# Kernel optimization log

Hardware: AMD Instinct MI355X
Metric: run time of the kernel (lower is better)

## Reference

```python
import jax, jax.numpy as jnp
import numpy as np

N_USER, N_ITEM, N_BUNDLE = 200000, 100000, 50000
EMBED_DIM = 128
B, L = 8192, 100  # batch of bundles, max items per bundle


def setup_inputs() -> dict:
    key = jax.random.key(0)
    ks = jax.random.split(key, 12)
    d, d2 = EMBED_DIM, 2 * EMBED_DIM
    x_u = jax.random.randint(ks[0], (B,), 0, N_USER)
    x_b = jax.random.randint(ks[1], (B,), 0, N_BUNDLE)
    items = jax.random.randint(ks[2], (B, L), 0, N_ITEM)
    # ragged bundle sizes in [10, L]; padded+masked form of the CSR gather
    lengths = jax.random.randint(ks[3], (B,), 10, L + 1)
    mask = jnp.arange(L)[None, :] < lengths[:, None]  # [B, L] bool
    return {
        "x_u": x_u,
        "x_b": x_b,
        "items": items,
        "mask": mask,
        "emb_u": jax.random.normal(ks[4], (N_USER, d), jnp.float32) * 0.1,
        "emb_i": jax.random.normal(ks[5], (N_ITEM, d), jnp.float32) * 0.1,
        "emb_b": jax.random.normal(ks[6], (N_BUNDLE, d), jnp.float32) * 0.1,
        "A": jax.random.normal(ks[7], (N_ITEM, d), jnp.float32) * 0.1,
        "fc1_w": jax.random.normal(ks[8], (d2, d2), jnp.float32) / np.sqrt(d2),
        "fc1_b": jnp.zeros((d2,), jnp.float32),
        "fc2_w": jax.random.normal(ks[9], (d2, d2), jnp.float32) / np.sqrt(d2),
        "fc2_b": jnp.zeros((d2,), jnp.float32),
        "out_w": jax.random.normal(ks[10], (1, d2), jnp.float32) / np.sqrt(d2),
        "out_b": jnp.zeros((1,), jnp.float32),
    }


def reference(x_u, x_b, items, mask, emb_u, emb_i, emb_b, A,
              fc1_w, fc1_b, fc2_w, fc2_b, out_w, out_b):
    # DAM.forward_bundle with the attention() per-bundle loop vectorized
    h_u = emb_u[x_u]                       # [B, d]
    h_b = emb_b[x_b]                       # [B, d]
    item_e = emb_i[items]                  # [B, L, d] ragged gather (padded)
    a_e = A[items]                         # [B, L, d]
    # w = softmax_l( sum_d e_u * A[item] ) per bundle, over valid items only
    scores = jnp.einsum('bd,bld->bl', h_u, a_e)
    scores = jnp.where(mask, scores, -jnp.inf)
    w = jax.nn.softmax(scores, axis=1)     # [B, L]
    h_x = jnp.einsum('bl,bld->bd', w, item_e)
    h = jnp.concatenate([h_u, h_b + h_x], axis=1)   # [B, 2d]
    h = jax.nn.leaky_relu(h @ fc1_w.T + fc1_b)
    h = jax.nn.leaky_relu(h @ fc2_w.T + fc2_b)
    return h @ out_w.T + out_b             # [B, 1]
```

## Files before the change

kernel.cpp:

```cpp
#include <hip/hip_runtime.h>
#include <hip/hip_bf16.h>

#define D   128
#define D2  256
#define XS  264
#define H1P 272

typedef short bf16x8 __attribute__((ext_vector_type(8)));
typedef float f32x4  __attribute__((ext_vector_type(4)));

__device__ __forceinline__ float bf2f(unsigned short u) {
    return __uint_as_float(((unsigned int)u) << 16);
}
__device__ __forceinline__ float bflo(unsigned int p) { return __uint_as_float(p << 16); }
__device__ __forceinline__ float bfhi(unsigned int p) { return __uint_as_float(p & 0xffff0000u); }
__device__ __forceinline__ unsigned short f2bf(float f) {
    __hip_bfloat16 h = __float2bfloat16(f);
    return *(unsigned short*)&h;
}

template<bool BF>
__device__ __forceinline__ float ld1(const void* p, size_t i) {
    if constexpr (BF) return bf2f(((const unsigned short*)p)[i]);
    else              return ((const float*)p)[i];
}

template<bool BF>
__device__ __forceinline__ void load8f(const void* p, size_t elem_off, float* r) {
    if constexpr (BF) {
        uint4 v = *(const uint4*)((const unsigned short*)p + elem_off);
        r[0]=bflo(v.x); r[1]=bfhi(v.x); r[2]=bflo(v.y); r[3]=bfhi(v.y);
        r[4]=bflo(v.z); r[5]=bfhi(v.z); r[6]=bflo(v.w); r[7]=bfhi(v.w);
    } else {
        const float4* q = (const float4*)((const float*)p + elem_off);
        float4 a = q[0], b = q[1];
        r[0]=a.x; r[1]=a.y; r[2]=a.z; r[3]=a.w;
        r[4]=b.x; r[5]=b.y; r[6]=b.z; r[7]=b.w;
    }
}

__device__ __forceinline__ void unpack8(uint4 v, float* r) {
    r[0]=bflo(v.x); r[1]=bfhi(v.x); r[2]=bflo(v.y); r[3]=bfhi(v.y);
    r[4]=bflo(v.z); r[5]=bfhi(v.z); r[6]=bflo(v.w); r[7]=bfhi(v.w);
}

__device__ __forceinline__ void store8bf(unsigned short* p, const float* r) {
    union { unsigned short u[8]; uint4 v; } pk;
    #pragma unroll
    for (int k = 0; k < 8; ++k) pk.u[k] = f2bf(r[k]);
    *(uint4*)p = pk.v;
}

__device__ __forceinline__ bool read_mask(const void* mask, int mmode, size_t i) {
    if (mmode == 0) return ((const int*)mask)[i] != 0;
    if (mmode == 1) return ((const unsigned char*)mask)[i] != 0;
    return ((const unsigned short*)mask)[i] != 0;
}

__device__ __forceinline__ bool probe_is_bf16(const unsigned int* probe) {
    const int lane = threadIdx.x & 63;
    int cnt = 0;
    #pragma unroll
    for (int i = 0; i < 4; ++i) {
        unsigned int e = (probe[lane + 64 * i] >> 7) & 0xffu;
        cnt += (e >= 90 && e < 130) ? 1 : 0;
    }
    #pragma unroll
    for (int o = 32; o; o >>= 1) cnt += __shfl_xor(cnt, o);
    return cnt >= 128;
}

template<bool BF>
__device__ __forceinline__ void attn_one_row(
    const int* __restrict__ x_u, const int* __restrict__ x_b,
    const int* __restrict__ items, const void* __restrict__ mask, int mmode,
    const void* __restrict__ emb_u, const void* __restrict__ emb_i,
    const void* __restrict__ emb_b, const void* __restrict__ Aw,
    unsigned short* __restrict__ x_row, int b, int L)
{
    const int lane = threadIdx.x & 63;
    const int xu = x_u[b];

    const int  c0 = (lane < L) ? lane : 0;
    int  i0 = items[(size_t)b * L + c0];
    bool v0 = (lane < L) && read_mask(mask, mmode, (size_t)b * L + c0);
    int  i1 = i0;
    bool v1 = false;
    if (64 + lane < L) {
        i1 = items[(size_t)b * L + 64 + lane];
        v1 = read_mask(mask, mmode, (size_t)b * L + 64 + lane);
    }
    const int len = __popcll(__ballot(v0)) + __popcll(__ballot(v1));

    const int g = lane >> 4, m16 = lane & 15;

    float hu8[8];
    load8f<BF>(emb_u, (size_t)xu * D + m16 * 8, hu8);

    auto get_id = [&](int p) -> int {
        const int idx = 4 * p + g;
        const int src = (idx < len) ? idx : 0;
        return (src < 64) ? __shfl(i0, src) : __shfl(i1, src - 64);
    };

    float esum = 0.f;
    float acc8[8];
    #pragma unroll
    for (int k = 0; k < 8; ++k) acc8[k] = 0.f;

    if constexpr (BF) {
        const unsigned short* AW = (const unsigned short*)Aw;
        const unsigned short* EI = (const unsigned short*)emb_i;
        for (int grp = 0; grp < 4; ++grp) {
            if (grp == 0 || grp * 32 < len) {
                uint4 ab[8], vb[8];
                #pragma unroll
                for (int q = 0; q < 8; ++q) {
                    const int id = get_id(grp * 8 + q);
                    ab[q] = *(const uint4*)(AW + (size_t)id * D + m16 * 8);
                    vb[q] = *(const uint4*)(EI + (size_t)id * D + m16 * 8);
                }
                #pragma unroll
                for (int q = 0; q < 8; ++q) {
                    float af[8];
                    unpack8(ab[q], af);
                    float s = 0.f;
                    #pragma unroll
                    for (int k = 0; k < 8; ++k) s += hu8[k] * af[k];
                    s += __shfl_xor(s, 1); s += __shfl_xor(s, 2);
                    s += __shfl_xor(s, 4); s += __shfl_xor(s, 8);
                    const int idx = 4 * (grp * 8 + q) + g;
                    const float e = (idx < len) ? __expf(s) : 0.f;
                    esum += e;
                    float vf[8];
                    unpack8(vb[q], vf);
                    #pragma unroll
                    for (int k = 0; k < 8; ++k) acc8[k] += e * vf[k];
                }
            }
        }
    } else {
        const int NP = (len + 3) >> 2;
        auto fetchf = [&](int p, float* a, float* v) {
            const int id = get_id(p);
            load8f<false>(Aw,    (size_t)id * D + m16 * 8, a);
            load8f<false>(emb_i, (size_t)id * D + m16 * 8, v);
        };
        float a0[8], u0[8], a1[8], u1[8];
        fetchf(0, a0, u0);
        if (1 < NP) fetchf(1, a1, u1);
        for (int p = 0; p < NP; ++p) {
            float ca[8], cv[8];
            #pragma unroll
            for (int k = 0; k < 8; ++k) { ca[k] = a0[k]; cv[k] = u0[k]; }
            #pragma unroll
            for (int k = 0; k < 8; ++k) { a0[k] = a1[k]; u0[k] = u1[k]; }
            if (p + 2 < NP) fetchf(p + 2, a1, u1);
            float s = 0.f;
            #pragma unroll
            for (int k = 0; k < 8; ++k) s += hu8[k] * ca[k];
            s += __shfl_xor(s, 1); s += __shfl_xor(s, 2);
            s += __shfl_xor(s, 4); s += __shfl_xor(s, 8);
            const int idx = 4 * p + g;
            const float e = (idx < len) ? __expf(s) : 0.f;
            esum += e;
            #pragma unroll
            for (int k = 0; k < 8; ++k) acc8[k] += e * cv[k];
        }
    }

    esum += __shfl_xor(esum, 16);
    esum += __shfl_xor(esum, 32);
    #pragma unroll
    for (int k = 0; k < 8; ++k) {
        acc8[k] += __shfl_xor(acc8[k], 16);
        acc8[k] += __shfl_xor(acc8[k], 32);
    }
    const float inv = (esum > 0.f) ? 1.f / esum : 0.f;

    if (g == 0) {
        if constexpr (BF) {
            uint4 raw = *(const uint4*)((const unsigned short*)emb_u
                                        + (size_t)xu * D + m16 * 8);
            *(uint4*)(x_row + m16 * 8) = raw;
        } else {
            float r[8];
            load8f<false>(emb_u, (size_t)xu * D + m16 * 8, r);
            store8bf(x_row + m16 * 8, r);
        }
        const int xb = x_b[b];
        float rb2[8], outv[8];
        load8f<BF>(emb_b, (size_t)xb * D + m16 * 8, rb2);
        #pragma unroll
        for (int k = 0; k < 8; ++k) outv[k] = rb2[k] + acc8[k] * inv;
        store8bf(x_row + D + m16 * 8, outv);
    }
}

template<bool BF>
__device__ __forceinline__ bf16x8 load_w8(const void* W, size_t off) {
    if constexpr (BF) {
        return *(const bf16x8*)((const unsigned short*)W + off);
    } else {
        const float* p = (const float*)W + off;
        float4 a = *(const float4*)p;
        float4 b = *(const float4*)(p + 4);
        bf16x8 r;
        r[0] = (short)f2bf(a.x); r[1] = (short)f2bf(a.y);
        r[2] = (short)f2bf(a.z); r[3] = (short)f2bf(a.w);
        r[4] = (short)f2bf(b.x); r[5] = (short)f2bf(b.y);
        r[6] = (short)f2bf(b.z); r[7] = (short)f2bf(b.w);
        return r;
    }
}

template<bool BF>
__device__ __forceinline__ void fused_body(
    const int* __restrict__ x_u, const int* __restrict__ x_b,
    const int* __restrict__ items, const void* __restrict__ mask, int mmode,
    const void* __restrict__ emb_u, const void* __restrict__ emb_i,
    const void* __restrict__ emb_b, const void* __restrict__ Aw,
    const void* __restrict__ fc1_w, const void* __restrict__ fc1_b,
    const void* __restrict__ fc2_w, const void* __restrict__ fc2_b,
    const void* __restrict__ out_w, const void* __restrict__ out_b,
    void* __restrict__ out, int L,
    unsigned short* x_s, unsigned short* h1_s, float (*po_s)[16])
{
    const int tid  = threadIdx.x;
    const int wave = tid >> 6;
    const int lane = tid & 63;
    const int l16  = lane & 15;
    const int quad = lane >> 4;
    const int mt   = blockIdx.x * 16;

    #pragma unroll
    for (int rr = 0; rr < 2; ++rr) {
        const int r = wave + rr * 8;
        attn_one_row<BF>(x_u, x_b, items, mask, mmode, emb_u, emb_i, emb_b, Aw,
                         &x_s[r * XS], mt + r, L);
    }
    __syncthreads();

    bf16x8 afrag[8];
    #pragma unroll
    for (int kc = 0; kc < 8; ++kc)
        afrag[kc] = *(const bf16x8*)&x_s[l16 * XS + quad * 8 + kc * 32];

    #pragma unroll
    for (int jj = 0; jj < 2; ++jj) {
        const int jt = wave * 2 + jj;
        const size_t bbase = (size_t)(jt * 16 + l16) * D2 + quad * 8;
        f32x4 acc = {0.f, 0.f, 0.f, 0.f};
        #pragma unroll
        for (int kc = 0; kc < 8; ++kc) {
            bf16x8 bfrag = load_w8<BF>(fc1_w, bbase + kc * 32);
            acc = __builtin_amdgcn_mfma_f32_16x16x32_bf16(afrag[kc], bfrag, acc, 0, 0, 0);
        }
        const int j  = jt * 16 + l16;
        const float bj = ld1<BF>(fc1_b, j);
        #pragma unroll
        for (int r = 0; r < 4; ++r) {
            float v = acc[r] + bj;
            v = v > 0.f ? v : 0.01f * v;
            h1_s[(quad * 4 + r) * H1P + j] = f2bf(v);
        }
    }
    __syncthreads();

    bf16x8 afrag2[8];
    #pragma unroll
    for (int kc = 0; kc < 8; ++kc)
        afrag2[kc] = *(const bf16x8*)&h1_s[l16 * H1P + quad * 8 + kc * 32];

    float po[4] = {0.f, 0.f, 0.f, 0.f};
    #pragma unroll
    for (int jj = 0; jj < 2; ++jj) {
        const int jt = wave * 2 + jj;
        const size_t bbase = (size_t)(jt * 16 + l16) * D2 + quad * 8;
        f32x4 acc = {0.f, 0.f, 0.f, 0.f};
        #pragma unroll
        for (int kc = 0; kc < 8; ++kc) {
            bf16x8 bfrag = load_w8<BF>(fc2_w, bbase + kc * 32);
            acc = __builtin_amdgcn_mfma_f32_16x16x32_bf16(afrag2[kc], bfrag, acc, 0, 0, 0);
        }
        const int j  = jt * 16 + l16;
        const float bj = ld1<BF>(fc2_b, j);
        const float wj = ld1<BF>(out_w, j);
        #pragma unroll
        for (int r = 0; r < 4; ++r) {
            float v = acc[r] + bj;
            v = v > 0.f ? v : 0.01f * v;
            po[r] += v * wj;
        }
    }
    #pragma unroll
    for (int r = 0; r < 4; ++r) {
        #pragma unroll
        for (int o = 1; o < 16; o <<= 1) po[r] += __shfl_xor(po[r], o);
    }
    if (l16 == 0) {
        #pragma unroll
        for (int r = 0; r < 4; ++r) po_s[wave][quad * 4 + r] = po[r];
    }
    __syncthreads();

    if (tid < 16) {
        float v = ld1<BF>(out_b, 0);
        #pragma unroll
        for (int w = 0; w < 8; ++w) v += po_s[w][tid];
        if constexpr (BF) ((unsigned short*)out)[mt + tid] = f2bf(v);
        else              ((float*)out)[mt + tid] = v;
    }
}

__global__ __launch_bounds__(512, 4) void fused_kernel(
    const int* x_u, const int* x_b, const int* items, const void* mask,
    const void* emb_u, const void* emb_i, const void* emb_b, const void* A,
    const void* fc1_w, const void* fc1_b, const void* fc2_w, const void* fc2_b,
    const void* out_w, const void* out_b, void* out, int L)
{
    __shared__ unsigned short x_s[16 * XS];
    __shared__ unsigned short h1_s[16 * H1P];
    __shared__ float po_s[8][16];

    const bool bf = probe_is_bf16((const unsigned int*)emb_u);
    const unsigned char* mb = (const unsigned char*)mask;
    const int mm = (mb[1] == 0) ? 0 : ((mb[0] == 1) ? 1 : 2);

    if (bf) fused_body<true >(x_u, x_b, items, mask, mm, emb_u, emb_i, emb_b, A,
                              fc1_w, fc1_b, fc2_w, fc2_b, out_w, out_b, out, L,
                              x_s, h1_s, po_s);
    else    fused_body<false>(x_u, x_b, items, mask, mm, emb_u, emb_i, emb_b, A,
                              fc1_w, fc1_b, fc2_w, fc2_b, out_w, out_b, out, L,
                              x_s, h1_s, po_s);
}

extern "C" void kernel_launch(void* const* d_in, const int* in_sizes, int n_in,
                              void* d_out, int out_size, void* d_ws, size_t ws_size,
                              hipStream_t stream) {
    const int*  x_u   = (const int*)d_in[0];
    const int*  x_b   = (const int*)d_in[1];
    const int*  items = (const int*)d_in[2];
    const void* mask  = d_in[3];
    const void* emb_u = d_in[4];
    const void* emb_i = d_in[5];
    const void* emb_b = d_in[6];
    const void* A     = d_in[7];
    const void* fc1_w = d_in[8];
    const void* fc1_b = d_in[9];
    const void* fc2_w = d_in[10];
    const void* fc2_b = d_in[11];
    const void* out_w = d_in[12];
    const void* out_b = d_in[13];

    const int B = in_sizes[0];
    const int L = in_sizes[2] / B;

    fused_kernel<<<B / 16, 512, 0, stream>>>(x_u, x_b, items, mask,
                                             emb_u, emb_i, emb_b, A,
                                             fc1_w, fc1_b, fc2_w, fc2_b,
                                             out_w, out_b, d_out, L);
}
```

Before: 299.9 us.

## Load-balance ragged attention by splitting bundles into 32-item slots across waves

Replaces the fixed two-rows-per-wave attention with a work list of 32-item slots. A prefix sum over the bundle lengths builds the list, waves take slots round-robin and write partial exp-sums and weighted sums to shared memory, and a reduction pass combines the partials per row. The aim is to remove wave imbalance from ragged bundle lengths and to issue more independent gathers at once. It costs extra shared memory (about 34KB more, which may reduce occupancy under launch bounds of 4 blocks), several extra barriers, and an unnormalized exp without max subtraction, which the old code also used.

Result: no change. 305.3 us (+1.8%).

```diff
diff --git a/kernel.cpp b/kernel.cpp
--- a/kernel.cpp
+++ b/kernel.cpp
@@ -1,10 +1,12 @@
 #include <hip/hip_runtime.h>
 #include <hip/hip_bf16.h>
 
-#define D   128
-#define D2  256
-#define XS  264
-#define H1P 272
+#define D    128
+#define D2   256
+#define XS   264
+#define H1P  272
+#define LMAX 128
+#define MAXSLOT 64
 
 typedef short bf16x8 __attribute__((ext_vector_type(8)));
 typedef float f32x4  __attribute__((ext_vector_type(4)));
@@ -68,133 +70,6 @@
     #pragma unroll
     for (int o = 32; o; o >>= 1) cnt += __shfl_xor(cnt, o);
     return cnt >= 128;
-}
-
-template<bool BF>
-__device__ __forceinline__ void attn_one_row(
-    const int* __restrict__ x_u, const int* __restrict__ x_b,
-    const int* __restrict__ items, const void* __restrict__ mask, int mmode,
-    const void* __restrict__ emb_u, const void* __restrict__ emb_i,
-    const void* __restrict__ emb_b, const void* __restrict__ Aw,
-    unsigned short* __restrict__ x_row, int b, int L)
-{
-    const int lane = threadIdx.x & 63;
-    const int xu = x_u[b];
-
-    const int  c0 = (lane < L) ? lane : 0;
-    int  i0 = items[(size_t)b * L + c0];
-    bool v0 = (lane < L) && read_mask(mask, mmode, (size_t)b * L + c0);
-    int  i1 = i0;
-    bool v1 = false;
-    if (64 + lane < L) {
-        i1 = items[(size_t)b * L + 64 + lane];
-        v1 = read_mask(mask, mmode, (size_t)b * L + 64 + lane);
-    }
-    const int len = __popcll(__ballot(v0)) + __popcll(__ballot(v1));
-
-    const int g = lane >> 4, m16 = lane & 15;
-
-    float hu8[8];
-    load8f<BF>(emb_u, (size_t)xu * D + m16 * 8, hu8);
-
-    auto get_id = [&](int p) -> int {
-        const int idx = 4 * p + g;
-        const int src = (idx < len) ? idx : 0;
-        return (src < 64) ? __shfl(i0, src) : __shfl(i1, src - 64);
-    };
-
-    float esum = 0.f;
-    float acc8[8];
-    #pragma unroll
-    for (int k = 0; k < 8; ++k) acc8[k] = 0.f;
-
-    if constexpr (BF) {
-        const unsigned short* AW = (const unsigned short*)Aw;
-        const unsigned short* EI = (const unsigned short*)emb_i;
-        for (int grp = 0; grp < 4; ++grp) {
-            if (grp == 0 || grp * 32 < len) {
-                uint4 ab[8], vb[8];
-                #pragma unroll
-                for (int q = 0; q < 8; ++q) {
-                    const int id = get_id(grp * 8 + q);
-                    ab[q] = *(const uint4*)(AW + (size_t)id * D + m16 * 8);
-                    vb[q] = *(const uint4*)(EI + (size_t)id * D + m16 * 8);
-                }
-                #pragma unroll
-                for (int q = 0; q < 8; ++q) {
-                    float af[8];
-                    unpack8(ab[q], af);
-                    float s = 0.f;
-                    #pragma unroll
-                    for (int k = 0; k < 8; ++k) s += hu8[k] * af[k];
-                    s += __shfl_xor(s, 1); s += __shfl_xor(s, 2);
-                    s += __shfl_xor(s, 4); s += __shfl_xor(s, 8);
-                    const int idx = 4 * (grp * 8 + q) + g;
-                    const float e = (idx < len) ? __expf(s) : 0.f;
-                    esum += e;
-                    float vf[8];
-                    unpack8(vb[q], vf);
-                    #pragma unroll
-                    for (int k = 0; k < 8; ++k) acc8[k] += e * vf[k];
-                }
-            }
-        }
-    } else {
-        const int NP = (len + 3) >> 2;
-        auto fetchf = [&](int p, float* a, float* v) {
-            const int id = get_id(p);
-            load8f<false>(Aw,    (size_t)id * D + m16 * 8, a);
-            load8f<false>(emb_i, (size_t)id * D + m16 * 8, v);
-        };
-        float a0[8], u0[8], a1[8], u1[8];
-        fetchf(0, a0, u0);
-        if (1 < NP) fetchf(1, a1, u1);
-        for (int p = 0; p < NP; ++p) {
-            float ca[8], cv[8];
-            #pragma unroll
-            for (int k = 0; k < 8; ++k) { ca[k] = a0[k]; cv[k] = u0[k]; }
-            #pragma unroll
-            for (int k = 0; k < 8; ++k) { a0[k] = a1[k]; u0[k] = u1[k]; }
-            if (p + 2 < NP) fetchf(p + 2, a1, u1);
-            float s = 0.f;
-            #pragma unroll
-            for (int k = 0; k < 8; ++k) s += hu8[k] * ca[k];
-            s += __shfl_xor(s, 1); s += __shfl_xor(s, 2);
-            s += __shfl_xor(s, 4); s += __shfl_xor(s, 8);
-            const int idx = 4 * p + g;
-            const float e = (idx < len) ? __expf(s) : 0.f;
-            esum += e;
-            #pragma unroll
-            for (int k = 0; k < 8; ++k) acc8[k] += e * cv[k];
-        }
-    }
-
-    esum += __shfl_xor(esum, 16);
-    esum += __shfl_xor(esum, 32);
-    #pragma unroll
-    for (int k = 0; k < 8; ++k) {
-        acc8[k] += __shfl_xor(acc8[k], 16);
-        acc8[k] += __shfl_xor(acc8[k], 32);
-    }
-    const float inv = (esum > 0.f) ? 1.f / esum : 0.f;
-
-    if (g == 0) {
-        if constexpr (BF) {
-            uint4 raw = *(const uint4*)((const unsigned short*)emb_u
-                                        + (size_t)xu * D + m16 * 8);
-            *(uint4*)(x_row + m16 * 8) = raw;
-        } else {
-            float r[8];
-            load8f<false>(emb_u, (size_t)xu * D + m16 * 8, r);
-            store8bf(x_row + m16 * 8, r);
-        }
-        const int xb = x_b[b];
-        float rb2[8], outv[8];
-        load8f<BF>(emb_b, (size_t)xb * D + m16 * 8, rb2);
-        #pragma unroll
-        for (int k = 0; k < 8; ++k) outv[k] = rb2[k] + acc8[k] * inv;
-        store8bf(x_row + D + m16 * 8, outv);
-    }
 }
 
 template<bool BF>
@@ -224,11 +99,15 @@
     const void* __restrict__ fc2_w, const void* __restrict__ fc2_b,
     const void* __restrict__ out_w, const void* __restrict__ out_b,
     void* __restrict__ out, int L,
+    int* it_s, float (*hu_s)[D], float (*part)[132],
+    int* len_s, int* pfx_s, unsigned char* srow_s, unsigned char* sgrp_s,
     unsigned short* x_s, unsigned short* h1_s, float (*po_s)[16])
 {
     const int tid  = threadIdx.x;
     const int wave = tid >> 6;
     const int lane = tid & 63;
+    const int g    = lane >> 4;
+    const int m16  = lane & 15;
     const int l16  = lane & 15;
     const int quad = lane >> 4;
     const int mt   = blockIdx.x * 16;
@@ -236,8 +115,172 @@
     #pragma unroll
     for (int rr = 0; rr < 2; ++rr) {
         const int r = wave + rr * 8;
-        attn_one_row<BF>(x_u, x_b, items, mask, mmode, emb_u, emb_i, emb_b, Aw,
-                         &x_s[r * XS], mt + r, L);
+        const int b = mt + r;
+        const int  c0 = (lane < L) ? lane : 0;
+        int  i0 = items[(size_t)b * L + c0];
+        bool v0 = (lane < L) && read_mask(mask, mmode, (size_t)b * L + c0);
+        int  i1 = 0;
+        bool v1 = false;
+        if (64 + lane < L) {
+            i1 = items[(size_t)b * L + 64 + lane];
+            v1 = read_mask(mask, mmode, (size_t)b * L + 64 + lane);
+        }
+        if (lane < L)       it_s[r * LMAX + lane]      = i0;
+        if (64 + lane < L && 64 + lane < LMAX) it_s[r * LMAX + 64 + lane] = i1;
+        int len = __popcll(__ballot(v0)) + __popcll(__ballot(v1));
+        if (len > LMAX) len = LMAX;
+        if (lane == 0) len_s[r] = len;
+
+        const int xu = x_u[b];
+        if (g == 0) {
+            float r8[8];
+            load8f<BF>(emb_u, (size_t)xu * D + m16 * 8, r8);
+            #pragma unroll
+            for (int k = 0; k < 8; ++k) hu_s[r][m16 * 8 + k] = r8[k];
+            if constexpr (BF) {
+                uint4 raw = *(const uint4*)((const unsigned short*)emb_u
+                                            + (size_t)xu * D + m16 * 8);
+                *(uint4*)(x_s + (size_t)r * XS + m16 * 8) = raw;
+            } else {
+                store8bf(x_s + (size_t)r * XS + m16 * 8, r8);
+            }
+        }
+    }
+    __syncthreads();
+
+    if (tid < 17) {
+        int s = 0;
+        for (int i = 0; i < tid; ++i) {
+            const int gi = (len_s[i] + 31) >> 5;
+            s += (gi < 4) ? gi : 4;
+        }
+        pfx_s[tid] = s;
+    }
+    __syncthreads();
+    const int nslots = pfx_s[16];
+    if (tid < nslots) {
+        int r = 0;
+        while (pfx_s[r + 1] <= tid) ++r;
+        srow_s[tid] = (unsigned char)r;
+        sgrp_s[tid] = (unsigned char)(tid - pfx_s[r]);
+    }
+    __syncthreads();
+
+    for (int k = wave; k < nslots; k += 8) {
+        const int row = srow_s[k];
+        const int grp = sgrp_s[k];
+        const int len = len_s[row];
+        const int* itr = &it_s[row * LMAX];
+
+        float hu8[8];
+        #pragma unroll
+        for (int j = 0; j < 8; ++j) hu8[j] = hu_s[row][m16 * 8 + j];
+
+        float esum = 0.f;
+        float acc8[8];
+        #pragma unroll
+        for (int j = 0; j < 8; ++j) acc8[j] = 0.f;
+
+        if constexpr (BF) {
+            const unsigned short* AW = (const unsigned short*)Aw;
+            const unsigned short* EI = (const unsigned short*)emb_i;
+            int idq[8];
+            #pragma unroll
+            for (int q = 0; q < 8; ++q) {
+                const int idx = grp * 32 + 4 * q + g;
+                idq[q] = itr[(idx < len) ? idx : 0];
+            }
+            uint4 ab[8], vb[8];
+            #pragma unroll
+            for (int q = 0; q < 8; ++q) {
+                ab[q] = *(const uint4*)(AW + (size_t)idq[q] * D + m16 * 8);
+                vb[q] = *(const uint4*)(EI + (size_t)idq[q] * D + m16 * 8);
+            }
+            #pragma unroll
+            for (int q = 0; q < 8; ++q) {
+                float af[8];
+                unpack8(ab[q], af);
+                float s = 0.f;
+                #pragma unroll
+                for (int j = 0; j < 8; ++j) s += hu8[j] * af[j];
+                s += __shfl_xor(s, 1); s += __shfl_xor(s, 2);
+                s += __shfl_xor(s, 4); s += __shfl_xor(s, 8);
+                const int idx = grp * 32 + 4 * q + g;
+                const float e = (idx < len) ? __expf(s) : 0.f;
+                esum += e;
+                float vf[8];
+                unpack8(vb[q], vf);
+                #pragma unroll
+                for (int j = 0; j < 8; ++j) acc8[j] += e * vf[j];
+            }
+        } else {
+            float a0[8], u0[8], a1[8], u1[8];
+            auto fetchf = [&](int q, float* a, float* v) {
+                const int idx = grp * 32 + 4 * q + g;
+                const int id = itr[(idx < len) ? idx : 0];
+                load8f<false>(Aw,    (size_t)id * D + m16 * 8, a);
+                load8f<false>(emb_i, (size_t)id * D + m16 * 8, v);
+            };
+            fetchf(0, a0, u0);
+            fetchf(1, a1, u1);
+            for (int q = 0; q < 8; ++q) {
+                float ca[8], cv[8];
+                #pragma unroll
+                for (int j = 0; j < 8; ++j) { ca[j] = a0[j]; cv[j] = u0[j]; }
+                #pragma unroll
+                for (int j = 0; j < 8; ++j) { a0[j] = a1[j]; u0[j] = u1[j]; }
+                if (q + 2 < 8) fetchf(q + 2, a1, u1);
+                float s = 0.f;
+                #pragma unroll
+                for (int j = 0; j < 8; ++j) s += hu8[j] * ca[j];
+                s += __shfl_xor(s, 1); s += __shfl_xor(s, 2);
+                s += __shfl_xor(s, 4); s += __shfl_xor(s, 8);
+                const int idx = grp * 32 + 4 * q + g;
+                const float e = (idx < len) ? __expf(s) : 0.f;
+                esum += e;
+                #pragma unroll
+                for (int j = 0; j < 8; ++j) acc8[j] += e * cv[j];
+            }
+        }
+
+        esum += __shfl_xor(esum, 16);
+        esum += __shfl_xor(esum, 32);
+        #pragma unroll
+        for (int j = 0; j < 8; ++j) {
+            acc8[j] += __shfl_xor(acc8[j], 16);
+            acc8[j] += __shfl_xor(acc8[j], 32);
+        }
+        if (g == 0) {
+            #pragma unroll
+            for (int j = 0; j < 8; ++j) part[k][m16 * 8 + j] = acc8[j];
+            if (m16 == 0) part[k][128] = esum;
+        }
+    }
+    __syncthreads();
+
+    if (g == 0) {
+        #pragma unroll
+        for (int rr = 0; rr < 2; ++rr) {
+            const int r = wave + rr * 8;
+            const int b = mt + r;
+            float at[8];
+            #pragma unroll
+            for (int j = 0; j < 8; ++j) at[j] = 0.f;
+            float es = 0.f;
+            const int k0 = pfx_s[r], k1 = pfx_s[r + 1];
+            for (int k = k0; k < k1; ++k) {
+                #pragma unroll
+                for (int j = 0; j < 8; ++j) at[j] += part[k][m16 * 8 + j];
+                es += part[k][128];
+            }
+            const float inv = (es > 0.f) ? 1.f / es : 0.f;
+            const int xb = x_b[b];
+            float rb2[8], outv[8];
+            load8f<BF>(emb_b, (size_t)xb * D + m16 * 8, rb2);
+            #pragma unroll
+            for (int j = 0; j < 8; ++j) outv[j] = rb2[j] + at[j] * inv;
+            store8bf(x_s + (size_t)r * XS + D + m16 * 8, outv);
+        }
     }
     __syncthreads();
 
@@ -319,6 +362,13 @@
     const void* fc1_w, const void* fc1_b, const void* fc2_w, const void* fc2_b,
     const void* out_w, const void* out_b, void* out, int L)
 {
+    __shared__ int   it_s[16 * LMAX];
+    __shared__ float hu_s[16][D];
+    __shared__ float part[MAXSLOT][132];
+    __shared__ int   len_s[16];
+    __shared__ int   pfx_s[17];
+    __shared__ unsigned char srow_s[MAXSLOT];
+    __shared__ unsigned char sgrp_s[MAXSLOT];
     __shared__ unsigned short x_s[16 * XS];
     __shared__ unsigned short h1_s[16 * H1P];
     __shared__ float po_s[8][16];
@@ -329,9 +379,11 @@
 
     if (bf) fused_body<true >(x_u, x_b, items, mask, mm, emb_u, emb_i, emb_b, A,
                               fc1_w, fc1_b, fc2_w, fc2_b, out_w, out_b, out, L,
+                              it_s, hu_s, part, len_s, pfx_s, srow_s, sgrp_s,
                               x_s, h1_s, po_s);
     else    fused_body<false>(x_u, x_b, items, mask, mm, emb_u, emb_i, emb_b, A,
                               fc1_w, fc1_b, fc2_w, fc2_b, out_w, out_b, out, L,
+                              it_s, hu_s, part, len_s, pfx_s, srow_s, sgrp_s,
                               x_s, h1_s, po_s);
 }
 
```

## Process four bundles per block with 256 threads instead of sixteen

Applied to the files above, without the earlier changes.

Each block now handles 4 bundle rows with 4 waves (one attention row per wave) instead of 16 rows across 8 waves, and the grid grows fourfold. The MFMA MLP stages pad the 16-row A tile with zeros, using only 4 valid rows, and each wave now covers 4 output column tiles instead of 2. The goal is more blocks and less per-block serialization in the gather-bound attention phase, so latency hides better. The cost is re-reading the fc1 and fc2 weights four times as often and wasting most of each MFMA on zero rows.

After: 392.4 us. +30.9%, slower.

```diff
diff --git a/kernel.cpp b/kernel.cpp
--- a/kernel.cpp
+++ b/kernel.cpp
@@ -68,6 +68,23 @@
     #pragma unroll
     for (int o = 32; o; o >>= 1) cnt += __shfl_xor(cnt, o);
     return cnt >= 128;
+}
+
+template<bool BF>
+__device__ __forceinline__ bf16x8 load_w8(const void* W, size_t off) {
+    if constexpr (BF) {
+        return *(const bf16x8*)((const unsigned short*)W + off);
+    } else {
+        const float* p = (const float*)W + off;
+        float4 a = *(const float4*)p;
+        float4 b = *(const float4*)(p + 4);
+        bf16x8 r;
+        r[0] = (short)f2bf(a.x); r[1] = (short)f2bf(a.y);
+        r[2] = (short)f2bf(a.z); r[3] = (short)f2bf(a.w);
+        r[4] = (short)f2bf(b.x); r[5] = (short)f2bf(b.y);
+        r[6] = (short)f2bf(b.z); r[7] = (short)f2bf(b.w);
+        return r;
+    }
 }
 
 template<bool BF>
@@ -198,23 +215,6 @@
 }
 
 template<bool BF>
-__device__ __forceinline__ bf16x8 load_w8(const void* W, size_t off) {
-    if constexpr (BF) {
-        return *(const bf16x8*)((const unsigned short*)W + off);
-    } else {
-        const float* p = (const float*)W + off;
-        float4 a = *(const float4*)p;
-        float4 b = *(const float4*)(p + 4);
-        bf16x8 r;
-        r[0] = (short)f2bf(a.x); r[1] = (short)f2bf(a.y);
-        r[2] = (short)f2bf(a.z); r[3] = (short)f2bf(a.w);
-        r[4] = (short)f2bf(b.x); r[5] = (short)f2bf(b.y);
-        r[6] = (short)f2bf(b.z); r[7] = (short)f2bf(b.w);
-        return r;
-    }
-}
-
-template<bool BF>
 __device__ __forceinline__ void fused_body(
     const int* __restrict__ x_u, const int* __restrict__ x_b,
     const int* __restrict__ items, const void* __restrict__ mask, int mmode,
@@ -224,31 +224,30 @@
     const void* __restrict__ fc2_w, const void* __restrict__ fc2_b,
     const void* __restrict__ out_w, const void* __restrict__ out_b,
     void* __restrict__ out, int L,
-    unsigned short* x_s, unsigned short* h1_s, float (*po_s)[16])
+    unsigned short (*x_s)[XS], unsigned short (*h1_s)[H1P], float (*po_s)[4])
 {
     const int tid  = threadIdx.x;
     const int wave = tid >> 6;
     const int lane = tid & 63;
     const int l16  = lane & 15;
     const int quad = lane >> 4;
-    const int mt   = blockIdx.x * 16;
-
-    #pragma unroll
-    for (int rr = 0; rr < 2; ++rr) {
-        const int r = wave + rr * 8;
-        attn_one_row<BF>(x_u, x_b, items, mask, mmode, emb_u, emb_i, emb_b, Aw,
-                         &x_s[r * XS], mt + r, L);
-    }
+    const int mt   = blockIdx.x * 4;
+
+    attn_one_row<BF>(x_u, x_b, items, mask, mmode, emb_u, emb_i, emb_b, Aw,
+                     x_s[wave], mt + wave, L);
     __syncthreads();
 
+    const bf16x8 zfrag = {0, 0, 0, 0, 0, 0, 0, 0};
+
     bf16x8 afrag[8];
     #pragma unroll
     for (int kc = 0; kc < 8; ++kc)
-        afrag[kc] = *(const bf16x8*)&x_s[l16 * XS + quad * 8 + kc * 32];
-
-    #pragma unroll
-    for (int jj = 0; jj < 2; ++jj) {
-        const int jt = wave * 2 + jj;
+        afrag[kc] = (l16 < 4) ? *(const bf16x8*)&x_s[l16][quad * 8 + kc * 32]
+                              : zfrag;
+
+    #pragma unroll
+    for (int jj = 0; jj < 4; ++jj) {
+        const int jt = wave * 4 + jj;
         const size_t bbase = (size_t)(jt * 16 + l16) * D2 + quad * 8;
         f32x4 acc = {0.f, 0.f, 0.f, 0.f};
         #pragma unroll
@@ -258,11 +257,13 @@
         }
         const int j  = jt * 16 + l16;
         const float bj = ld1<BF>(fc1_b, j);
-        #pragma unroll
-        for (int r = 0; r < 4; ++r) {
-            float v = acc[r] + bj;
-            v = v > 0.f ? v : 0.01f * v;
-            h1_s[(quad * 4 + r) * H1P + j] = f2bf(v);
+        if (quad == 0) {
+            #pragma unroll
+            for (int r = 0; r < 4; ++r) {
+                float v = acc[r] + bj;
+                v = v > 0.f ? v : 0.01f * v;
+                h1_s[r][j] = f2bf(v);
+            }
         }
     }
     __syncthreads();
@@ -270,12 +271,13 @@
     bf16x8 afrag2[8];
     #pragma unroll
     for (int kc = 0; kc < 8; ++kc)
-        afrag2[kc] = *(const bf16x8*)&h1_s[l16 * H1P + quad * 8 + kc * 32];
+        afrag2[kc] = (l16 < 4) ? *(const bf16x8*)&h1_s[l16][quad * 8 + kc * 32]
+                               : zfrag;
 
     float po[4] = {0.f, 0.f, 0.f, 0.f};
     #pragma unroll
-    for (int jj = 0; jj < 2; ++jj) {
-        const int jt = wave * 2 + jj;
+    for (int jj = 0; jj < 4; ++jj) {
+        const int jt = wave * 4 + jj;
         const size_t bbase = (size_t)(jt * 16 + l16) * D2 + quad * 8;
         f32x4 acc = {0.f, 0.f, 0.f, 0.f};
         #pragma unroll
@@ -298,30 +300,29 @@
         #pragma unroll
         for (int o = 1; o < 16; o <<= 1) po[r] += __shfl_xor(po[r], o);
     }
-    if (l16 == 0) {
-        #pragma unroll
-        for (int r = 0; r < 4; ++r) po_s[wave][quad * 4 + r] = po[r];
+    if (lane == 0) {
+        #pragma unroll
+        for (int r = 0; r < 4; ++r) po_s[wave][r] = po[r];
     }
     __syncthreads();
 
-    if (tid < 16) {
-        float v = ld1<BF>(out_b, 0);
-        #pragma unroll
-        for (int w = 0; w < 8; ++w) v += po_s[w][tid];
+    if (tid < 4) {
+        const float v = po_s[0][tid] + po_s[1][tid] + po_s[2][tid] + po_s[3][tid]
+                      + ld1<BF>(out_b, 0);
         if constexpr (BF) ((unsigned short*)out)[mt + tid] = f2bf(v);
         else              ((float*)out)[mt + tid] = v;
     }
 }
 
-__global__ __launch_bounds__(512, 4) void fused_kernel(
+__global__ __launch_bounds__(256) void fused_kernel(
     const int* x_u, const int* x_b, const int* items, const void* mask,
     const void* emb_u, const void* emb_i, const void* emb_b, const void* A,
     const void* fc1_w, const void* fc1_b, const void* fc2_w, const void* fc2_b,
     const void* out_w, const void* out_b, void* out, int L)
 {
-    __shared__ unsigned short x_s[16 * XS];
-    __shared__ unsigned short h1_s[16 * H1P];
-    __shared__ float po_s[8][16];
+    __shared__ unsigned short x_s[4][XS];
+    __shared__ unsigned short h1_s[4][H1P];
+    __shared__ float po_s[4][4];
 
     const bool bf = probe_is_bf16((const unsigned int*)emb_u);
     const unsigned char* mb = (const unsigned char*)mask;
@@ -356,8 +357,8 @@
     const int B = in_sizes[0];
     const int L = in_sizes[2] / B;
 
-    fused_kernel<<<B / 16, 512, 0, stream>>>(x_u, x_b, items, mask,
-                                             emb_u, emb_i, emb_b, A,
-                                             fc1_w, fc1_b, fc2_w, fc2_b,
-                                             out_w, out_b, d_out, L);
-}
+    fused_kernel<<<B / 4, 256, 0, stream>>>(x_u, x_b, items, mask,
+                                            emb_u, emb_i, emb_b, A,
+                                            fc1_w, fc1_b, fc2_w, fc2_b,
+                                            out_w, out_b, d_out, L);
+}
```
